# Performance work log

Hardware: AMD Instinct MI355X
Metric: run time of the kernel (lower is better)

The kernel has to match this reference:

```python
import jax, jax.numpy as jnp
import numpy as np

DIM = 2048; KV_RANK = 512; Q_RANK = 768; H = 16
D_NR = 128; D_R = 64; D_V = 128
B = 8; L = 32; MAX_T = 4096; START = MAX_T - L
QK_DIM = D_NR + D_R
SCALE = 1.0 / float(np.sqrt(QK_DIM))
EPS = 1.1920929e-07  # torch.finfo(float32).eps (nn.RMSNorm default)
ROPE_BASE = 10000.0


def rms_norm(x, w):
    return x * jax.lax.rsqrt(jnp.mean(x * x, axis=-1, keepdims=True) + EPS) * w


def apply_rope(x, cos, sin):
    # x: (b, l, h, d) with d even; cos/sin: (l, d//2) -> complex multiply on pairs
    b, l, h, d = x.shape
    xp = x.reshape(b, l, h, d // 2, 2)
    xr, xi = xp[..., 0], xp[..., 1]
    c = cos[None, :, None, :]
    s = sin[None, :, None, :]
    return jnp.stack([xr * c - xi * s, xr * s + xi * c], axis=-1).reshape(b, l, h, d)


def setup_inputs() -> dict:
    key = jax.random.key(0)
    ks = jax.random.split(key, 9)
    w = 0.02
    # rotary angles for absolute positions START..START+L-1
    inv_freq = 1.0 / (ROPE_BASE ** (np.arange(0, D_R, 2, dtype=np.float32) / D_R))  # (32,)
    pos = np.arange(START, START + L, dtype=np.float32)
    ang = pos[:, None] * inv_freq[None, :]  # (L, 32)
    # causal mask over full cache: query i sits at absolute position START+i
    t = jnp.arange(MAX_T)[None, :]
    qpos = START + jnp.arange(L)[:, None]
    mask = jnp.where(t <= qpos, 0.0, -1e30).astype(jnp.float32)  # (L, MAX_T)
    return {
        "x": jax.random.normal(ks[0], (B, L, DIM), dtype=jnp.float32),
        "start_pos": START,
        "freq_cos": jnp.asarray(np.cos(ang), dtype=jnp.float32),
        "freq_sin": jnp.asarray(np.sin(ang), dtype=jnp.float32),
        "mask": mask,
        "kv_latent_cache": jax.random.normal(ks[1], (B, MAX_T, KV_RANK), dtype=jnp.float32) * 0.05,
        "k_rope_cache": jax.random.normal(ks[2], (B, MAX_T, D_R), dtype=jnp.float32) * 0.05,
        "w_kv_down": jax.random.normal(ks[3], (KV_RANK + D_R, DIM), dtype=jnp.float32) * w,
        "w_q_down": jax.random.normal(ks[4], (Q_RANK, DIM), dtype=jnp.float32) * w,
        "rms_q_w": jnp.ones((Q_RANK,), dtype=jnp.float32),
        "w_q_up": jax.random.normal(ks[5], (H * QK_DIM, Q_RANK), dtype=jnp.float32) * w,
        "w_kv_up": jax.random.normal(ks[6], (H * (D_NR + D_V), KV_RANK), dtype=jnp.float32) * w,
        "w_out": jax.random.normal(ks[7], (DIM, H * D_V), dtype=jnp.float32) * w,
    }


def reference(x, start_pos, freq_cos, freq_sin, mask, kv_latent_cache, k_rope_cache,
              w_kv_down, w_q_down, rms_q_w, w_q_up, w_kv_up, w_out):
    b, l, _ = x.shape
    end_pos = start_pos + l
    # query path: down-proj -> RMSNorm -> up-proj (NOTE: module's rms_norm_kv is unused)
    q = rms_norm(x @ w_q_down.T, rms_q_w) @ w_q_up.T
    q = q.reshape(b, l, H, QK_DIM)
    q_nrope, q_rope = q[..., :D_NR], q[..., D_NR:]
    q_rope = apply_rope(q_rope, freq_cos, freq_sin)
    # latent kv path
    kv = x @ w_kv_down.T  # (b, l, KV_RANK + D_R)
    kv_latent, k_rope = kv[..., :KV_RANK], kv[..., KV_RANK:]
    k_rope = apply_rope(k_rope[:, :, None, :], freq_cos, freq_sin)[:, :, 0, :]
    # scatter-write into caches, then read prefix [:end_pos]
    kvc = kv_latent_cache.at[:, start_pos:end_pos].set(kv_latent)[:, :end_pos]  # (b, t, k)
    krc = k_rope_cache.at[:, start_pos:end_pos].set(k_rope)[:, :end_pos]        # (b, t, r)
    # weight absorption
    w_up = w_kv_up.reshape(H, D_NR + D_V, KV_RANK)
    q_abs = jnp.einsum('blhd,hdk->blhk', q_nrope, w_up[:, :D_NR])
    scores = (jnp.einsum('blhk,btk->blht', q_abs, kvc)
              + jnp.einsum('blhr,btr->blht', q_rope, krc)) * SCALE
    scores = scores + mask[None, :, None, :]
    p = jax.nn.softmax(scores, axis=-1)
    o = jnp.einsum('blht,btk->blhk', p, kvc)
    o = jnp.einsum('blhk,hdk->blhd', o, w_up[:, D_NR:])
    return o.reshape(b, l, H * D_V) @ w_out.T
```

## Files before the change

### kernel.cpp

```cpp
#include <hip/hip_runtime.h>
#include <math.h>

#define DIMX 2048
#define KV_RANK 512
#define Q_RANK 768
#define NH 16
#define D_NR 128
#define D_R 64
#define D_V 128
#define NB 8
#define NL 32
#define MAX_T 4096
#define STARTP (MAX_T - NL)
#define QK_DIM (D_NR + D_R)
#define ATT_SCALE 0.07216878364870323f
#define RMS_EPS 1.1920929e-07f

typedef unsigned short u16;
typedef __attribute__((ext_vector_type(4))) unsigned short u16x4;
typedef __attribute__((ext_vector_type(8))) short short8;
typedef __attribute__((ext_vector_type(4))) float f32x4;

#define GLOBAL_AS __attribute__((address_space(1)))
#define LDS_AS __attribute__((address_space(3)))

#define NDOWN 1344
#define DPART ((long long)256 * NDOWN)

__device__ inline u16 f2b(float f) {
    union { float f; unsigned u; } v; v.f = f;
    unsigned r = (v.u + 0x7fffu + ((v.u >> 16) & 1u)) >> 16;
    return (u16)r;
}
__device__ inline float b2f(u16 u) {
    union { unsigned u; float f; } v; v.u = ((unsigned)u) << 16; return v.f;
}

template<int BM, int BN, int OUTMODE, bool GSWZ>
__global__ __launch_bounds__(256) void gemm_mfma(
    const u16* __restrict__ A, const u16* __restrict__ B, void* __restrict__ Cv,
    float* __restrict__ rs,
    int K, int lda, int ldb, int ldc,
    long long sA1, long long sA2, long long sB1, long long sB2,
    long long sC1, long long sC2, int nb2)
{
    constexpr int MFR = BM / 32;
    constexpr int NFR = BN / 32;
    int bx = blockIdx.x, by = blockIdx.y, bz = blockIdx.z;
    if (GSWZ) {
        int flat = bx + gridDim.x * (by + gridDim.y * bz);
        int nwg = gridDim.x * gridDim.y * gridDim.z;
        int lf = (flat & 7) * (nwg >> 3) + (flat >> 3);
        bx = lf % gridDim.x;
        int r = lf / gridDim.x;
        by = r % gridDim.y;
        bz = r / gridDim.y;
    }
    const int z1 = bz / nb2, z2 = bz % nb2;
    A += z1 * sA1 + z2 * sA2;
    B += z1 * sB1 + z2 * sB2;

    const int m0 = by * BM;
    const int n0 = bx * BN;
    const int tid = threadIdx.x;
    const int lane = tid & 63;
    const int wid = tid >> 6;
    const int wm = wid >> 1, wn = wid & 1;
    const int l15 = lane & 15;
    const int l4  = lane >> 4;

    __shared__ __align__(16) u16 As[BM * 32];
    __shared__ __align__(16) u16 Bs[BN * 32];

    f32x4 acc[MFR][NFR];
    #pragma unroll
    for (int i = 0; i < MFR; ++i)
        #pragma unroll
        for (int j = 0; j < NFR; ++j)
            acc[i][j] = (f32x4)0.0f;

    constexpr int nA = BM / 16;
    constexpr int nB = BN / 16;

    for (int k0 = 0; k0 < K; k0 += 32) {
        #pragma unroll
        for (int j = 0; j < nA / 4 + 1; ++j) {
            int jj = wid + j * 4;
            if (jj < nA) {
                int c = jj * 64 + lane;
                int row = c >> 2;
                int ksg = (c & 3) ^ ((row >> 1) & 3);
                const u16* src = A + (long long)(m0 + row) * lda + k0 + ksg * 8;
                u16* dst = &As[jj * 512];
                __builtin_amdgcn_global_load_lds((const GLOBAL_AS void*)src,
                                                 (LDS_AS void*)dst, 16, 0, 0);
            }
        }
        #pragma unroll
        for (int j = 0; j < nB / 4 + 1; ++j) {
            int jj = wid + j * 4;
            if (jj < nB) {
                int c = jj * 64 + lane;
                int row = c >> 2;
                int ksg = (c & 3) ^ ((row >> 1) & 3);
                const u16* src = B + (long long)(n0 + row) * ldb + k0 + ksg * 8;
                u16* dst = &Bs[jj * 512];
                __builtin_amdgcn_global_load_lds((const GLOBAL_AS void*)src,
                                                 (LDS_AS void*)dst, 16, 0, 0);
            }
        }
        __syncthreads();

        short8 a[MFR], b[NFR];
        #pragma unroll
        for (int mf = 0; mf < MFR; ++mf) {
            int row = wm * 16 * MFR + mf * 16 + l15;
            int ksl = l4 ^ ((row >> 1) & 3);
            a[mf] = *(const short8*)&As[row * 32 + ksl * 8];
        }
        #pragma unroll
        for (int nf = 0; nf < NFR; ++nf) {
            int row = wn * 16 * NFR + nf * 16 + l15;
            int ksl = l4 ^ ((row >> 1) & 3);
            b[nf] = *(const short8*)&Bs[row * 32 + ksl * 8];
        }
        #pragma unroll
        for (int mf = 0; mf < MFR; ++mf)
            #pragma unroll
            for (int nf = 0; nf < NFR; ++nf)
                acc[mf][nf] = __builtin_amdgcn_mfma_f32_16x16x32_bf16(
                    a[mf], b[nf], acc[mf][nf], 0, 0, 0);
        __syncthreads();
    }

    if (OUTMODE == 2) {
        u16* C = (u16*)Cv + z1 * sC1 + z2 * sC2;
        float rowp[MFR][4];
        #pragma unroll
        for (int mf = 0; mf < MFR; ++mf)
            #pragma unroll
            for (int r = 0; r < 4; ++r)
                rowp[mf][r] = 0.f;
        #pragma unroll
        for (int mf = 0; mf < MFR; ++mf) {
            #pragma unroll
            for (int nf = 0; nf < NFR; ++nf) {
                int r0 = m0 + wm * 16 * MFR + mf * 16 + l4 * 4;
                int c0 = n0 + wn * 16 * NFR + nf * 16 + l15;
                #pragma unroll
                for (int r = 0; r < 4; ++r) {
                    int row = r0 + r;
                    int vlen = STARTP + (row & 31) + 1;
                    float p = (c0 < vlen) ? __expf(acc[mf][nf][r] * ATT_SCALE) : 0.f;
                    u16 pb = f2b(p);
                    C[(long long)row * ldc + c0] = pb;
                    rowp[mf][r] += b2f(pb);
                }
            }
        }
        #pragma unroll
        for (int mf = 0; mf < MFR; ++mf)
            #pragma unroll
            for (int r = 0; r < 4; ++r) {
                float v = rowp[mf][r];
                v += __shfl_xor(v, 1);
                v += __shfl_xor(v, 2);
                v += __shfl_xor(v, 4);
                v += __shfl_xor(v, 8);
                if (l15 == 0) {
                    int row = m0 + wm * 16 * MFR + mf * 16 + l4 * 4 + r;
                    atomicAdd(&rs[z1 * 512 + row], v);
                }
            }
    } else if (OUTMODE == 1) {
        u16* C = (u16*)Cv + z1 * sC1 + z2 * sC2;
        #pragma unroll
        for (int mf = 0; mf < MFR; ++mf)
            #pragma unroll
            for (int nf = 0; nf < NFR; ++nf) {
                int r0 = m0 + wm * 16 * MFR + mf * 16 + l4 * 4;
                int c0 = n0 + wn * 16 * NFR + nf * 16 + l15;
                #pragma unroll
                for (int r = 0; r < 4; ++r)
                    C[(long long)(r0 + r) * ldc + c0] = f2b(acc[mf][nf][r]);
            }
    } else {
        float* C = (float*)Cv + z1 * sC1 + z2 * sC2;
        #pragma unroll
        for (int mf = 0; mf < MFR; ++mf)
            #pragma unroll
            for (int nf = 0; nf < NFR; ++nf) {
                int r0 = m0 + wm * 16 * MFR + mf * 16 + l4 * 4;
                int c0 = n0 + wn * 16 * NFR + nf * 16 + l15;
                #pragma unroll
                for (int r = 0; r < 4; ++r)
                    C[(long long)(r0 + r) * ldc + c0] = acc[mf][nf][r];
            }
    }
}

struct Segs {
    const float* src[6];
    u16* dst[6];
    int n4[6];
};
__global__ __launch_bounds__(256) void f2b_multi(Segs s)
{
    int seg = blockIdx.y;
    int i = blockIdx.x * 256 + threadIdx.x;
    if (i >= s.n4[seg]) return;
    float4 v = ((const float4*)s.src[seg])[i];
    u16x4 o = { f2b(v.x), f2b(v.y), f2b(v.z), f2b(v.w) };
    ((u16x4*)s.dst[seg])[i] = o;
}

__global__ __launch_bounds__(256) void rs_zero(float* __restrict__ rs)
{
    int i = blockIdx.x * 256 + threadIdx.x;
    float4 z = { 0.f, 0.f, 0.f, 0.f };
    ((float4*)rs)[i] = z;
}

__global__ __launch_bounds__(256) void rms_reduce(const float* __restrict__ part,
                                                  const float* __restrict__ w,
                                                  u16* __restrict__ outb)
{
    const int row = blockIdx.x;
    const int tid = threadIdx.x;
    __shared__ float red[256];
    float val[3];
    float s = 0.f;
    #pragma unroll
    for (int j = 0; j < 3; ++j) {
        int i = tid + j * 256;
        long long off = (long long)row * NDOWN + i;
        float v = part[off] + part[DPART + off] + part[2 * DPART + off] + part[3 * DPART + off];
        val[j] = v;
        s += v * v;
    }
    red[tid] = s; __syncthreads();
    for (int off = 128; off > 0; off >>= 1) {
        if (tid < off) red[tid] += red[tid + off];
        __syncthreads();
    }
    float scale = rsqrtf(red[0] / (float)Q_RANK + RMS_EPS);
    u16* ob = outb + (long long)row * Q_RANK;
    #pragma unroll
    for (int j = 0; j < 3; ++j) {
        int i = tid + j * 256;
        ob[i] = f2b(val[j] * scale * w[i]);
    }
}

__global__ __launch_bounds__(256) void wuT_kernel(const float* __restrict__ w,
                                                  u16* __restrict__ outp)
{
    __shared__ u16 T[64][65];
    const int h = blockIdx.z;
    const int y0 = blockIdx.y * 64;
    const int x0 = blockIdx.x * 64;
    const int tid = threadIdx.x;
    #pragma unroll
    for (int i = 0; i < 16; ++i) {
        int lin = i * 256 + tid;
        int r = lin >> 6, c = lin & 63;
        T[c][r] = f2b(w[((long long)h * 256 + y0 + r) * 512 + x0 + c]);
    }
    __syncthreads();
    #pragma unroll
    for (int i = 0; i < 16; ++i) {
        int lin = i * 256 + tid;
        int r = lin >> 6, c = lin & 63;
        outp[((long long)h * 512 + x0 + r) * 128 + y0 + c] = T[r][c];
    }
}

__global__ __launch_bounds__(256) void bcat_new_reduce(const float* __restrict__ part,
                                                       const float* __restrict__ fc,
                                                       const float* __restrict__ fs,
                                                       u16* __restrict__ bcat)
{
    const int bl = blockIdx.x;
    const int b = bl >> 5, l = bl & 31;
    const int t = threadIdx.x;
    if (t >= 144) return;
    long long off = (long long)bl * NDOWN + 768 + 4 * t;
    float4 v0 = *(const float4*)(part + off);
    float4 v1 = *(const float4*)(part + DPART + off);
    float4 v2 = *(const float4*)(part + 2 * DPART + off);
    float4 v3 = *(const float4*)(part + 3 * DPART + off);
    float4 v = { v0.x + v1.x + v2.x + v3.x, v0.y + v1.y + v2.y + v3.y,
                 v0.z + v1.z + v2.z + v3.z, v0.w + v1.w + v2.w + v3.w };
    u16* dst = bcat + ((long long)b * MAX_T + STARTP + l) * 576;
    if (t < 128) {
        u16x4 o = { f2b(v.x), f2b(v.y), f2b(v.z), f2b(v.w) };
        ((u16x4*)dst)[t] = o;
    } else {
        int g = t - 128;
        float c0 = fc[l * 32 + 2 * g],     s0 = fs[l * 32 + 2 * g];
        float c1 = fc[l * 32 + 2 * g + 1], s1 = fs[l * 32 + 2 * g + 1];
        u16x4 o = { f2b(v.x * c0 - v.y * s0), f2b(v.x * s0 + v.y * c0),
                    f2b(v.z * c1 - v.w * s1), f2b(v.z * s1 + v.w * c1) };
        *(u16x4*)(dst + 512 + 4 * g) = o;
    }
}

__global__ __launch_bounds__(256) void prep_cache(const float* __restrict__ kvc,
                                                  const float* __restrict__ krc,
                                                  u16* __restrict__ bcat,
                                                  u16* __restrict__ kvcT)
{
    const int b = blockIdx.z;
    const int t0 = blockIdx.y * 64;
    const int tid = threadIdx.x;

    if (blockIdx.x == 8) {
        #pragma unroll
        for (int i = 0; i < 4; ++i) {
            int lin = i * 256 + tid;
            int r = lin >> 4, c4 = lin & 15;
            int t = t0 + r;
            if (t >= STARTP) continue;
            float4 v = ((const float4*)(krc + ((long long)b * MAX_T + t) * D_R))[c4];
            u16x4 o = { f2b(v.x), f2b(v.y), f2b(v.z), f2b(v.w) };
            *(u16x4*)(bcat + ((long long)b * MAX_T + t) * 576 + 512 + 4 * c4) = o;
        }
        return;
    }

    __shared__ u16 T[64 * 64];
    const int k0 = blockIdx.x * 64;

    #pragma unroll
    for (int i = 0; i < 4; ++i) {
        int lin = i * 256 + tid;
        int r = lin >> 4, c4 = lin & 15;
        int t = t0 + r;
        u16x4 o;
        if (t < STARTP) {
            float4 v = *(const float4*)(kvc + ((long long)b * MAX_T + t) * KV_RANK + k0 + 4 * c4);
            o.x = f2b(v.x); o.y = f2b(v.y); o.z = f2b(v.z); o.w = f2b(v.w);
            *(u16x4*)(bcat + ((long long)b * MAX_T + t) * 576 + k0 + 4 * c4) = o;
        } else {
            o = *(const u16x4*)(bcat + ((long long)b * MAX_T + t) * 576 + k0 + 4 * c4);
        }
        int tg = r >> 2, te = r & 3;
        int col = ((tg ^ c4) << 2) + te;
        #pragma unroll
        for (int j = 0; j < 4; ++j)
            T[(4 * c4 + j) * 64 + col] = o[j];
    }
    __syncthreads();

    u16* outp = kvcT + ((long long)b * KV_RANK + k0) * MAX_T + t0;
    #pragma unroll
    for (int i = 0; i < 4; ++i) {
        int lin = i * 256 + tid;
        int k = lin >> 4, c4 = lin & 15;
        u16x4 v = *(const u16x4*)&T[k * 64 + ((c4 ^ (k >> 2)) << 2)];
        *(u16x4*)(outp + (long long)k * MAX_T + 4 * c4) = v;
    }
}

__global__ __launch_bounds__(256) void rope_q(const u16* __restrict__ qb,
                                              const float* __restrict__ fc,
                                              const float* __restrict__ fs,
                                              u16* __restrict__ qprimeb)
{
    int idx = blockIdx.x * 256 + threadIdx.x;
    int i = idx & 31;
    int h = (idx >> 5) & (NH - 1);
    int l = (idx >> 9) & (NL - 1);
    int b = idx >> 14;
    const u16* src = qb + (long long)(b * NL + l) * 3072 + h * QK_DIM + D_NR + 2 * i;
    float xr = b2f(src[0]), xi = b2f(src[1]);
    float c = fc[l * 32 + i], s = fs[l * 32 + i];
    u16* dst = qprimeb + ((long long)(b * NH + h) * NL + l) * 576 + 512 + 2 * i;
    dst[0] = f2b(xr * c - xi * s);
    dst[1] = f2b(xr * s + xi * c);
}

__global__ __launch_bounds__(256) void reduce_pv(const float* __restrict__ part,
                                                 const float* __restrict__ rs,
                                                 u16* __restrict__ o_hb)
{
    int idx = blockIdx.x * 256 + threadIdx.x;
    int b = idx >> 16;
    int i4 = idx & 65535;
    int m = i4 >> 7;
    const float* p = part + (long long)b * 1048576 + 4 * i4;
    float4 v0 = *(const float4*)p;
    float4 v1 = *(const float4*)(p + 262144);
    float4 v2 = *(const float4*)(p + 524288);
    float4 v3 = *(const float4*)(p + 786432);
    float inv = 1.0f / rs[b * 512 + m];
    u16x4 o = { f2b((v0.x + v1.x + v2.x + v3.x) * inv),
                f2b((v0.y + v1.y + v2.y + v3.y) * inv),
                f2b((v0.z + v1.z + v2.z + v3.z) * inv),
                f2b((v0.w + v1.w + v2.w + v3.w) * inv) };
    ((u16x4*)(o_hb + (long long)b * 262144))[i4] = o;
}

__global__ __launch_bounds__(256) void reduce_out(const float* __restrict__ part,
                                                  float* __restrict__ out)
{
    int idx = blockIdx.x * 256 + threadIdx.x;
    const float* p = part + 4 * (long long)idx;
    float4 v0 = *(const float4*)p;
    float4 v1 = *(const float4*)(p + 524288);
    float4 v2 = *(const float4*)(p + 1048576);
    float4 v3 = *(const float4*)(p + 1572864);
    float4 o = { v0.x + v1.x + v2.x + v3.x, v0.y + v1.y + v2.y + v3.y,
                 v0.z + v1.z + v2.z + v3.z, v0.w + v1.w + v2.w + v3.w };
    ((float4*)out)[idx] = o;
}

extern "C" void kernel_launch(void* const* d_in, const int* in_sizes, int n_in,
                              void* d_out, int out_size, void* d_ws, size_t ws_size,
                              hipStream_t stream)
{
    const float* x        = (const float*)d_in[0];
    const float* fc       = (const float*)d_in[2];
    const float* fs       = (const float*)d_in[3];
    const float* kvc      = (const float*)d_in[5];
    const float* krc      = (const float*)d_in[6];
    const float* w_kv_down= (const float*)d_in[7];
    const float* w_q_down = (const float*)d_in[8];
    const float* rms_q_w  = (const float*)d_in[9];
    const float* w_q_up   = (const float*)d_in[10];
    const float* w_kv_up  = (const float*)d_in[11];
    const float* w_out    = (const float*)d_in[12];
    float* out            = (float*)d_out;

    float* down_part = (float*)d_ws;
    float* rs      = down_part + 1376256;
    u16* pb        = (u16*)(rs + 4096);
    u16* base      = pb + 16777216;
    u16* xb      = base;                 base += 524288;
    u16* qdb     = base;                 base += 196608;
    u16* qb      = base;                 base += 786432;
    u16* qprimeb = base;                 base += 2359296;
    u16* wqkv_b  = base;                 base += 2752512;
    u16* wqu_b   = base;                 base += 2359296;
    u16* wkvu_b  = base;                 base += 2097152;
    u16* wout_b  = base;                 base += 4194304;
    u16* wuT     = base;                 base += 1048576;
    u16* bcat    = base;                 base += 18874368;
    u16* kvcT    = base;                 base += 16777216;
    u16* o_hb    = base;                 base += 2097152;
    u16* o_upb   = base;                 base += 524288;
    float* pv_part  = (float*)bcat;
    float* out_part = (float*)kvcT;

    Segs segs;
    segs.src[0] = x;         segs.dst[0] = xb;                  segs.n4[0] = 131072;
    segs.src[1] = w_q_down;  segs.dst[1] = wqkv_b;              segs.n4[1] = 393216;
    segs.src[2] = w_q_up;    segs.dst[2] = wqu_b;               segs.n4[2] = 589824;
    segs.src[3] = w_kv_down; segs.dst[3] = wqkv_b + 768 * 2048; segs.n4[3] = 294912;
    segs.src[4] = w_kv_up;   segs.dst[4] = wkvu_b;              segs.n4[4] = 524288;
    segs.src[5] = w_out;     segs.dst[5] = wout_b;              segs.n4[5] = 1048576;
    f2b_multi<<<dim3(4096, 6), 256, 0, stream>>>(segs);

    rs_zero<<<4, 256, 0, stream>>>(rs);
    wuT_kernel<<<dim3(8, 2, 16), 256, 0, stream>>>(w_kv_up, wuT);

    gemm_mfma<32, 64, 0, true><<<dim3(21, 8, 4), 256, 0, stream>>>(
        xb, wqkv_b, down_part, nullptr, 512, 2048, 2048, NDOWN,
        0LL, 512LL, 0LL, 512LL, 0LL, DPART, 4);
    rms_reduce<<<256, 256, 0, stream>>>(down_part, rms_q_w, qdb);
    gemm_mfma<32, 64, 1, true><<<dim3(48, 8, 1), 256, 0, stream>>>(
        qdb, wqu_b, qb, nullptr, 768, 768, 768, 3072, 0, 0, 0, 0, 0, 0, 1);
    bcat_new_reduce<<<256, 256, 0, stream>>>(down_part, fc, fs, bcat);
    prep_cache<<<dim3(9, 64, 8), 256, 0, stream>>>(kvc, krc, bcat, kvcT);

    gemm_mfma<32, 128, 1, true><<<dim3(4, 1, 128), 256, 0, stream>>>(
        qb, wuT, qprimeb, nullptr, 128, 3072, 128, 576,
        98304LL, 192LL, 0LL, 65536LL, 294912LL, 18432LL, 16);
    rope_q<<<512, 256, 0, stream>>>(qb, fc, fs, qprimeb);

    gemm_mfma<128, 128, 2, true><<<dim3(32, 4, 8), 256, 0, stream>>>(
        qprimeb, bcat, pb, rs, 576, 576, 576, 4096,
        294912LL, 0LL, 2359296LL, 0LL, 2097152LL, 0LL, 1);
    gemm_mfma<128, 128, 0, true><<<dim3(4, 4, 32), 256, 0, stream>>>(
        pb, kvcT, pv_part, nullptr, 1024, 4096, 4096, 512,
        2097152LL, 1024LL, 2097152LL, 1024LL, 1048576LL, 262144LL, 4);
    reduce_pv<<<2048, 256, 0, stream>>>(pv_part, rs, o_hb);

    gemm_mfma<32, 64, 1, true><<<dim3(2, 1, 128), 256, 0, stream>>>(
        o_hb, wkvu_b + 128 * 512, o_upb, nullptr, 512, 512, 512, 2048,
        262144LL, 16384LL, 0LL, 131072LL, 65536LL, 128LL, 16);
    gemm_mfma<32, 64, 0, true><<<dim3(32, 8, 4), 256, 0, stream>>>(
        o_upb, wout_b, out_part, nullptr, 512, 2048, 2048, 2048,
        0LL, 512LL, 0LL, 512LL, 0LL, 524288LL, 4);
    reduce_out<<<512, 256, 0, stream>>>(out_part, out);
}
```

Baseline: 323.4 us.

## Double-buffer GEMM LDS tiles with priority hints and widen cache-prep stores

The bf16 MFMA GEMM now double-buffers its A/B LDS tiles, prefetching the next K-slice with global_load_lds while the current slice is computed. This removes one barrier per iteration and raises wave priority around the MFMA block. The cache-prep kernel is also changed to process 8 elements per thread with 16-byte stores instead of 4 with 8-byte stores. The cost is doubled LDS usage per block, which may lower occupancy.

Result: no change. 317.3 us (-1.9%).

```diff
diff --git a/kernel.cpp b/kernel.cpp
--- a/kernel.cpp
+++ b/kernel.cpp
@@ -18,6 +18,7 @@
 
 typedef unsigned short u16;
 typedef __attribute__((ext_vector_type(4))) unsigned short u16x4;
+typedef __attribute__((ext_vector_type(8))) unsigned short u16x8;
 typedef __attribute__((ext_vector_type(8))) short short8;
 typedef __attribute__((ext_vector_type(4))) float f32x4;
 
@@ -69,20 +70,13 @@
     const int l15 = lane & 15;
     const int l4  = lane >> 4;
 
-    __shared__ __align__(16) u16 As[BM * 32];
-    __shared__ __align__(16) u16 Bs[BN * 32];
-
-    f32x4 acc[MFR][NFR];
-    #pragma unroll
-    for (int i = 0; i < MFR; ++i)
-        #pragma unroll
-        for (int j = 0; j < NFR; ++j)
-            acc[i][j] = (f32x4)0.0f;
+    __shared__ __align__(16) u16 As[2][BM * 32];
+    __shared__ __align__(16) u16 Bs[2][BN * 32];
 
     constexpr int nA = BM / 16;
     constexpr int nB = BN / 16;
 
-    for (int k0 = 0; k0 < K; k0 += 32) {
+    auto stage = [&](int buf, int k0) {
         #pragma unroll
         for (int j = 0; j < nA / 4 + 1; ++j) {
             int jj = wid + j * 4;
@@ -91,9 +85,8 @@
                 int row = c >> 2;
                 int ksg = (c & 3) ^ ((row >> 1) & 3);
                 const u16* src = A + (long long)(m0 + row) * lda + k0 + ksg * 8;
-                u16* dst = &As[jj * 512];
                 __builtin_amdgcn_global_load_lds((const GLOBAL_AS void*)src,
-                                                 (LDS_AS void*)dst, 16, 0, 0);
+                                                 (LDS_AS void*)&As[buf][jj * 512], 16, 0, 0);
             }
         }
         #pragma unroll
@@ -104,33 +97,48 @@
                 int row = c >> 2;
                 int ksg = (c & 3) ^ ((row >> 1) & 3);
                 const u16* src = B + (long long)(n0 + row) * ldb + k0 + ksg * 8;
-                u16* dst = &Bs[jj * 512];
                 __builtin_amdgcn_global_load_lds((const GLOBAL_AS void*)src,
-                                                 (LDS_AS void*)dst, 16, 0, 0);
+                                                 (LDS_AS void*)&Bs[buf][jj * 512], 16, 0, 0);
             }
         }
+    };
+
+    f32x4 acc[MFR][NFR];
+    #pragma unroll
+    for (int i = 0; i < MFR; ++i)
+        #pragma unroll
+        for (int j = 0; j < NFR; ++j)
+            acc[i][j] = (f32x4)0.0f;
+
+    const int nk = K >> 5;
+    stage(0, 0);
+    int cur = 0;
+    for (int ki = 0; ki < nk; ++ki) {
         __syncthreads();
+        if (ki + 1 < nk) stage(cur ^ 1, (ki + 1) << 5);
 
         short8 a[MFR], b[NFR];
         #pragma unroll
         for (int mf = 0; mf < MFR; ++mf) {
             int row = wm * 16 * MFR + mf * 16 + l15;
             int ksl = l4 ^ ((row >> 1) & 3);
-            a[mf] = *(const short8*)&As[row * 32 + ksl * 8];
+            a[mf] = *(const short8*)&As[cur][row * 32 + ksl * 8];
         }
         #pragma unroll
         for (int nf = 0; nf < NFR; ++nf) {
             int row = wn * 16 * NFR + nf * 16 + l15;
             int ksl = l4 ^ ((row >> 1) & 3);
-            b[nf] = *(const short8*)&Bs[row * 32 + ksl * 8];
-        }
+            b[nf] = *(const short8*)&Bs[cur][row * 32 + ksl * 8];
+        }
+        __builtin_amdgcn_s_setprio(1);
         #pragma unroll
         for (int mf = 0; mf < MFR; ++mf)
             #pragma unroll
             for (int nf = 0; nf < NFR; ++nf)
                 acc[mf][nf] = __builtin_amdgcn_mfma_f32_16x16x32_bf16(
                     a[mf], b[nf], acc[mf][nf], 0, 0, 0);
-        __syncthreads();
+        __builtin_amdgcn_s_setprio(0);
+        cur ^= 1;
     }
 
     if (OUTMODE == 2) {
@@ -316,14 +324,17 @@
 
     if (blockIdx.x == 8) {
         #pragma unroll
-        for (int i = 0; i < 4; ++i) {
+        for (int i = 0; i < 2; ++i) {
             int lin = i * 256 + tid;
-            int r = lin >> 4, c4 = lin & 15;
+            int r = lin >> 3, c8 = lin & 7;
             int t = t0 + r;
             if (t >= STARTP) continue;
-            float4 v = ((const float4*)(krc + ((long long)b * MAX_T + t) * D_R))[c4];
-            u16x4 o = { f2b(v.x), f2b(v.y), f2b(v.z), f2b(v.w) };
-            *(u16x4*)(bcat + ((long long)b * MAX_T + t) * 576 + 512 + 4 * c4) = o;
+            const float* src = krc + ((long long)b * MAX_T + t) * D_R + 8 * c8;
+            float4 v0 = *(const float4*)src;
+            float4 v1 = *(const float4*)(src + 4);
+            u16x8 o = { f2b(v0.x), f2b(v0.y), f2b(v0.z), f2b(v0.w),
+                        f2b(v1.x), f2b(v1.y), f2b(v1.z), f2b(v1.w) };
+            *(u16x8*)(bcat + ((long long)b * MAX_T + t) * 576 + 512 + 8 * c8) = o;
         }
         return;
     }
@@ -332,33 +343,46 @@
     const int k0 = blockIdx.x * 64;
 
     #pragma unroll
-    for (int i = 0; i < 4; ++i) {
+    for (int i = 0; i < 2; ++i) {
         int lin = i * 256 + tid;
-        int r = lin >> 4, c4 = lin & 15;
+        int r = lin >> 3, c8 = lin & 7;
         int t = t0 + r;
-        u16x4 o;
+        u16x4 oa, ob;
         if (t < STARTP) {
-            float4 v = *(const float4*)(kvc + ((long long)b * MAX_T + t) * KV_RANK + k0 + 4 * c4);
-            o.x = f2b(v.x); o.y = f2b(v.y); o.z = f2b(v.z); o.w = f2b(v.w);
-            *(u16x4*)(bcat + ((long long)b * MAX_T + t) * 576 + k0 + 4 * c4) = o;
+            const float* src = kvc + ((long long)b * MAX_T + t) * KV_RANK + k0 + 8 * c8;
+            float4 v0 = *(const float4*)src;
+            float4 v1 = *(const float4*)(src + 4);
+            oa[0] = f2b(v0.x); oa[1] = f2b(v0.y); oa[2] = f2b(v0.z); oa[3] = f2b(v0.w);
+            ob[0] = f2b(v1.x); ob[1] = f2b(v1.y); ob[2] = f2b(v1.z); ob[3] = f2b(v1.w);
+            u16x8 o = { oa[0], oa[1], oa[2], oa[3], ob[0], ob[1], ob[2], ob[3] };
+            *(u16x8*)(bcat + ((long long)b * MAX_T + t) * 576 + k0 + 8 * c8) = o;
         } else {
-            o = *(const u16x4*)(bcat + ((long long)b * MAX_T + t) * 576 + k0 + 4 * c4);
+            const u16* s = bcat + ((long long)b * MAX_T + t) * 576 + k0 + 8 * c8;
+            oa = *(const u16x4*)s;
+            ob = *(const u16x4*)(s + 4);
         }
         int tg = r >> 2, te = r & 3;
-        int col = ((tg ^ c4) << 2) + te;
-        #pragma unroll
-        for (int j = 0; j < 4; ++j)
-            T[(4 * c4 + j) * 64 + col] = o[j];
+        int c4a = 2 * c8, c4b = 2 * c8 + 1;
+        int cola = ((tg ^ c4a) << 2) + te;
+        int colb = ((tg ^ c4b) << 2) + te;
+        #pragma unroll
+        for (int j = 0; j < 4; ++j) {
+            T[(4 * c4a + j) * 64 + cola] = oa[j];
+            T[(4 * c4b + j) * 64 + colb] = ob[j];
+        }
     }
     __syncthreads();
 
     u16* outp = kvcT + ((long long)b * KV_RANK + k0) * MAX_T + t0;
     #pragma unroll
-    for (int i = 0; i < 4; ++i) {
+    for (int i = 0; i < 2; ++i) {
         int lin = i * 256 + tid;
-        int k = lin >> 4, c4 = lin & 15;
-        u16x4 v = *(const u16x4*)&T[k * 64 + ((c4 ^ (k >> 2)) << 2)];
-        *(u16x4*)(outp + (long long)k * MAX_T + 4 * c4) = v;
+        int k = lin >> 3, c8 = lin & 7;
+        int s = k >> 2;
+        u16x4 va = *(const u16x4*)&T[k * 64 + (((2 * c8) ^ s) << 2)];
+        u16x4 vb = *(const u16x4*)&T[k * 64 + (((2 * c8 + 1) ^ s) << 2)];
+        u16x8 o = { va[0], va[1], va[2], va[3], vb[0], vb[1], vb[2], vb[3] };
+        *(u16x8*)(outp + (long long)k * MAX_T + 8 * c8) = o;
     }
 }
 
```
